# Optimization experiments

Hardware: AMD Instinct MI355X
Metric: run time of the kernel (lower is better)

The kernel has to match this reference:

```python
import jax, jax.numpy as jnp
import numpy as np
from jax import lax

WIN = 11
SIGMA = 1.5


def _gaussian_kernel2d(win_size, channels, dtype):
    g = jnp.arange(win_size, dtype=dtype) - win_size // 2
    g = jnp.exp(-(g ** 2) / (2.0 * SIGMA ** 2))
    g = g / g.sum()
    k2 = jnp.einsum('i,j->ij', g, g)
    return jnp.broadcast_to(k2, (channels, 1, win_size, win_size))


def setup_inputs() -> dict:
    key = jax.random.key(0)
    k1, k2 = jax.random.split(key)
    B, C, H, W = 8, 19, 512, 512
    pred = jax.random.normal(k1, (B, C, H, W), dtype=jnp.float32)
    target = jax.random.randint(k2, (B, H, W), 0, C, dtype=jnp.int64)
    return {"pred": pred, "target": target}


def reference(pred, target):
    B, C, H, W = pred.shape
    win = min(H, W, WIN)
    p = jax.nn.softmax(pred, axis=1)
    t = jax.nn.one_hot(target, C, dtype=p.dtype).transpose(0, 3, 1, 2)  # [B,C,H,W]
    kernel = _gaussian_kernel2d(win, C, p.dtype)

    def dwconv(x):  # depthwise valid conv over all classes at once
        return lax.conv_general_dilated(x, kernel, (1, 1), 'VALID',
                                        feature_group_count=C)

    mu1 = dwconv(p)
    mu2 = dwconv(t)
    mu12 = mu1 * mu2
    mu1sq = mu1 * mu1
    mu2sq = mu2 * mu2
    var1 = dwconv(p * p) - mu1sq
    var2 = dwconv(t * t) - mu2sq
    covar = dwconv(p * t) - mu12

    L = 1.0
    c1 = (0.01 * L) ** 2
    c2 = (0.03 * L) ** 2
    cs = (2.0 * covar + c2) / (var1 + var2 + c2)
    ss = (2.0 * mu12 + c1) / (mu1sq + mu2sq + c1) * cs  # [B,C,H',W']

    ss = ss.reshape(B, C, -1).mean(axis=-1)  # per (batch, class) SSIM
    ss = jax.nn.relu(ss)  # nonnegative=True
    # loss = mean over classes of (1 - mean over batch of ss) == 1 - mean(ss)
    return 1.0 - ss.mean()
```

## Files before the change

kernel.cpp:

```cpp
#include <hip/hip_runtime.h>

namespace {

constexpr int B = 8, C = 19, H = 512, W = 512;
constexpr int OH = 502, OW = 502;
constexpr int HW = H * W;
constexpr int TH = 32, TW = 64;
constexpr int IH = TH + 10, IW = TW + 10;

__device__ constexpr float G[11] = {
    0.00102838f, 0.00759876f, 0.03600077f, 0.10936070f, 0.21300553f,
    0.26601173f,
    0.21300553f, 0.10936070f, 0.03600077f, 0.00759876f, 0.00102838f};

__global__ __launch_bounds__(256) void denom_kernel(
    const float* __restrict__ pred, const int* __restrict__ target,
    float* __restrict__ rs, unsigned char* __restrict__ t8,
    float* __restrict__ accum) {
  int idx = blockIdx.x * 256 + threadIdx.x;
  if (blockIdx.x == 0 && threadIdx.x < B * C) accum[threadIdx.x] = 0.0f;
  if (idx >= B * HW) return;
  int b = idx / HW;
  int px = idx - b * HW;
  const float* pp = pred + (size_t)b * C * HW + px;
  float s = 0.0f;
#pragma unroll
  for (int c = 0; c < C; ++c) s += __expf(pp[c * HW]);
  rs[idx] = 1.0f / s;
  t8[idx] = (unsigned char)target[idx];
}

__global__ __launch_bounds__(256) void ssim_kernel(
    const float* __restrict__ pred, const float* __restrict__ rs,
    const unsigned char* __restrict__ t8, float* __restrict__ accum) {
  __shared__ float sRS[IH][IW];
  __shared__ unsigned char sT[IH][IW];
  __shared__ float sP[IH][IW];
  __shared__ float sH[4][IH][TW];
  __shared__ float red[4];

  const int x0 = blockIdx.x * TW;
  const int y0 = blockIdx.y * TH;
  const int b = blockIdx.z;
  const int ow = min(TW, OW - x0);
  const int oh = min(TH, OH - y0);
  const int iw = ow + 10;
  const int ih = oh + 10;
  const int tid = threadIdx.x;

  for (int i = tid; i < ih * iw; i += 256) {
    int r = i / iw, col = i - r * iw;
    int g = b * HW + (y0 + r) * W + (x0 + col);
    sRS[r][col] = rs[g];
    sT[r][col] = t8[g];
  }
  __syncthreads();

  for (int c = 0; c < C; ++c) {
    const float* pc = pred + (size_t)(b * C + c) * HW;
    for (int i = tid; i < ih * iw; i += 256) {
      int r = i / iw, col = i - r * iw;
      sP[r][col] = __expf(pc[(y0 + r) * W + (x0 + col)]) * sRS[r][col];
    }
    __syncthreads();

    for (int i = tid; i < ih * TW; i += 256) {
      int r = i >> 6;
      int col = i & 63;
      if (col < ow) {
        float hp = 0.f, hp2 = 0.f, hpt = 0.f, ht = 0.f;
#pragma unroll
        for (int j = 0; j < 11; ++j) {
          float v = sP[r][col + j];
          float tf = (sT[r][col + j] == (unsigned char)c) ? 1.0f : 0.0f;
          float gj = G[j];
          hp += gj * v;
          hp2 += gj * v * v;
          hpt += gj * v * tf;
          ht += gj * tf;
        }
        sH[0][r][col] = hp;
        sH[1][r][col] = hp2;
        sH[2][r][col] = hpt;
        sH[3][r][col] = ht;
      }
    }
    __syncthreads();

    float acc = 0.0f;
    for (int i = tid; i < TH * TW; i += 256) {
      int r = i >> 6;
      int col = i & 63;
      if (r < oh && col < ow) {
        float mu1 = 0.f, dp2 = 0.f, dpt = 0.f, mu2 = 0.f;
#pragma unroll
        for (int j = 0; j < 11; ++j) {
          float gj = G[j];
          mu1 += gj * sH[0][r + j][col];
          dp2 += gj * sH[1][r + j][col];
          dpt += gj * sH[2][r + j][col];
          mu2 += gj * sH[3][r + j][col];
        }
        float mu12 = mu1 * mu2;
        float var1 = dp2 - mu1 * mu1;
        float var2 = mu2 - mu2 * mu2;
        float covar = dpt - mu12;
        const float c1 = 1e-4f, c2 = 9e-4f;
        float cs = (2.0f * covar + c2) / (var1 + var2 + c2);
        float ssv = (2.0f * mu12 + c1) / (mu1 * mu1 + mu2 * mu2 + c1) * cs;
        acc += ssv;
      }
    }

    for (int off = 32; off > 0; off >>= 1) acc += __shfl_down(acc, off);
    if ((tid & 63) == 0) red[tid >> 6] = acc;
    __syncthreads();
    if (tid == 0)
      atomicAdd(&accum[b * C + c], red[0] + red[1] + red[2] + red[3]);
  }
}

__global__ __launch_bounds__(256) void finish_kernel(
    const float* __restrict__ accum, float* __restrict__ out) {
  __shared__ float red[4];
  int tid = threadIdx.x;
  float v = 0.0f;
  if (tid < B * C) {
    float m = accum[tid] * (1.0f / (float)(OH * OW));
    v = m > 0.0f ? m : 0.0f;
  }
  for (int off = 32; off > 0; off >>= 1) v += __shfl_down(v, off);
  if ((tid & 63) == 0) red[tid >> 6] = v;
  __syncthreads();
  if (tid == 0) out[0] = 1.0f - (red[0] + red[1] + red[2] + red[3]) /
                                    (float)(B * C);
}

}

extern "C" void kernel_launch(void* const* d_in, const int* in_sizes, int n_in,
                              void* d_out, int out_size, void* d_ws,
                              size_t ws_size, hipStream_t stream) {
  const float* pred = (const float*)d_in[0];
  const int* target = (const int*)d_in[1];
  float* out = (float*)d_out;

  float* rs = (float*)d_ws;
  unsigned char* t8 = (unsigned char*)d_ws + (size_t)B * HW * sizeof(float);
  float* accum = (float*)((char*)d_ws + (size_t)B * HW * 5);

  denom_kernel<<<(B * HW + 255) / 256, 256, 0, stream>>>(pred, target, rs, t8,
                                                         accum);
  dim3 grid((OW + TW - 1) / TW, (OH + TH - 1) / TH, B);
  ssim_kernel<<<grid, 256, 0, stream>>>(pred, rs, t8, accum);
  finish_kernel<<<1, 256, 0, stream>>>(accum, out);
}
```

Measured before the change: 689.2 us.

## Restructure SSIM into register vertical pass, shared horizontal pass, class-split grid

The vertical Gaussian pass now runs in registers: each thread loads an 18-row column strip of pred and keeps rs/target values resident across classes. Only the four vertically filtered maps go through shared memory, and a register-blocked horizontal pass computes 7 outputs per thread. The grid is split four ways over class groups to raise parallelism, the denominator kernel is vectorized with float4/int4, and per-wave atomics replace the block reduction. The cost is a 64-column input tile producing 54 outputs, so more halo reloads, plus higher register pressure under the launch bound of 4 blocks.

```diff
diff --git a/kernel.cpp b/kernel.cpp
--- a/kernel.cpp
+++ b/kernel.cpp
@@ -5,8 +5,13 @@
 constexpr int B = 8, C = 19, H = 512, W = 512;
 constexpr int OH = 502, OW = 502;
 constexpr int HW = H * W;
-constexpr int TH = 32, TW = 64;
-constexpr int IH = TH + 10, IW = TW + 10;
+
+constexpr int TH = 32;
+constexpr int TW = 54;
+constexpr int IW = 64;
+constexpr int RPT = 8;
+constexpr int NJ = RPT + 10;
+constexpr int LW = 68;
 
 __device__ constexpr float G[11] = {
     0.00102838f, 0.00759876f, 0.03600077f, 0.10936070f, 0.21300553f,
@@ -17,106 +22,145 @@
     const float* __restrict__ pred, const int* __restrict__ target,
     float* __restrict__ rs, unsigned char* __restrict__ t8,
     float* __restrict__ accum) {
-  int idx = blockIdx.x * 256 + threadIdx.x;
+  int tid = blockIdx.x * 256 + threadIdx.x;
   if (blockIdx.x == 0 && threadIdx.x < B * C) accum[threadIdx.x] = 0.0f;
-  if (idx >= B * HW) return;
-  int b = idx / HW;
-  int px = idx - b * HW;
-  const float* pp = pred + (size_t)b * C * HW + px;
-  float s = 0.0f;
-#pragma unroll
-  for (int c = 0; c < C; ++c) s += __expf(pp[c * HW]);
-  rs[idx] = 1.0f / s;
-  t8[idx] = (unsigned char)target[idx];
-}
-
-__global__ __launch_bounds__(256) void ssim_kernel(
+  int p4 = tid * 4;
+  int b = p4 / HW;
+  int px = p4 - b * HW;
+  const float4* pp = (const float4*)(pred + (size_t)b * C * HW + px);
+  float4 s = {0.f, 0.f, 0.f, 0.f};
+#pragma unroll
+  for (int c = 0; c < C; ++c) {
+    float4 v = pp[c * (HW / 4)];
+    s.x += __expf(v.x);
+    s.y += __expf(v.y);
+    s.z += __expf(v.z);
+    s.w += __expf(v.w);
+  }
+  float4 r;
+  r.x = 1.0f / s.x;
+  r.y = 1.0f / s.y;
+  r.z = 1.0f / s.z;
+  r.w = 1.0f / s.w;
+  ((float4*)rs)[tid] = r;
+  int4 t = ((const int4*)target)[tid];
+  uchar4 tc;
+  tc.x = (unsigned char)t.x;
+  tc.y = (unsigned char)t.y;
+  tc.z = (unsigned char)t.z;
+  tc.w = (unsigned char)t.w;
+  ((uchar4*)t8)[tid] = tc;
+}
+
+__global__ __launch_bounds__(256, 4) void ssim_kernel(
     const float* __restrict__ pred, const float* __restrict__ rs,
     const unsigned char* __restrict__ t8, float* __restrict__ accum) {
-  __shared__ float sRS[IH][IW];
-  __shared__ unsigned char sT[IH][IW];
-  __shared__ float sP[IH][IW];
-  __shared__ float sH[4][IH][TW];
-  __shared__ float red[4];
-
+  __shared__ float vOut[4][TH][LW];
+
+  const int tid = threadIdx.x;
   const int x0 = blockIdx.x * TW;
   const int y0 = blockIdx.y * TH;
-  const int b = blockIdx.z;
+  const int z = blockIdx.z;
+  const int b = z >> 2;
+  const int c0 = (z & 3) * 5;
+  const int c1 = min(c0 + 5, C);
   const int ow = min(TW, OW - x0);
   const int oh = min(TH, OH - y0);
-  const int iw = ow + 10;
-  const int ih = oh + 10;
-  const int tid = threadIdx.x;
-
-  for (int i = tid; i < ih * iw; i += 256) {
-    int r = i / iw, col = i - r * iw;
-    int g = b * HW + (y0 + r) * W + (x0 + col);
-    sRS[r][col] = rs[g];
-    sT[r][col] = t8[g];
-  }
-  __syncthreads();
-
-  for (int c = 0; c < C; ++c) {
+
+  const int col = tid & 63;
+  const int rg = tid >> 6;
+  const int gc = min(x0 + col, W - 1);
+  const int rbase = y0 + rg * RPT;
+
+  float rsv[NJ];
+  int tv[NJ];
+#pragma unroll
+  for (int j = 0; j < NJ; ++j) {
+    int r = min(rbase + j, H - 1);
+    int o = b * HW + r * W + gc;
+    rsv[j] = rs[o];
+    tv[j] = t8[o];
+  }
+
+  const int prow = tid >> 3;
+  const int cg = tid & 7;
+  const int cbase = cg * 7;
+
+  for (int c = c0; c < c1; ++c) {
+    __syncthreads();
+
     const float* pc = pred + (size_t)(b * C + c) * HW;
-    for (int i = tid; i < ih * iw; i += 256) {
-      int r = i / iw, col = i - r * iw;
-      sP[r][col] = __expf(pc[(y0 + r) * W + (x0 + col)]) * sRS[r][col];
+    float aP[RPT] = {}, aP2[RPT] = {}, aPT[RPT] = {}, aT[RPT] = {};
+#pragma unroll
+    for (int j = 0; j < NJ; ++j) {
+      int r = min(rbase + j, H - 1);
+      float p = __expf(pc[r * W + gc]) * rsv[j];
+      float p2 = p * p;
+      bool hit = (tv[j] == c);
+      float tf = hit ? 1.0f : 0.0f;
+      float pt = hit ? p : 0.0f;
+#pragma unroll
+      for (int o = 0; o < RPT; ++o) {
+        int g = j - o;
+        if (g >= 0 && g < 11) {
+          float gw = G[g];
+          aP[o] = fmaf(gw, p, aP[o]);
+          aP2[o] = fmaf(gw, p2, aP2[o]);
+          aPT[o] = fmaf(gw, pt, aPT[o]);
+          aT[o] = fmaf(gw, tf, aT[o]);
+        }
+      }
+    }
+#pragma unroll
+    for (int o = 0; o < RPT; ++o) {
+      int r = rg * RPT + o;
+      vOut[0][r][col] = aP[o];
+      vOut[1][r][col] = aP2[o];
+      vOut[2][r][col] = aPT[o];
+      vOut[3][r][col] = aT[o];
     }
     __syncthreads();
 
-    for (int i = tid; i < ih * TW; i += 256) {
-      int r = i >> 6;
-      int col = i & 63;
-      if (col < ow) {
-        float hp = 0.f, hp2 = 0.f, hpt = 0.f, ht = 0.f;
-#pragma unroll
-        for (int j = 0; j < 11; ++j) {
-          float v = sP[r][col + j];
-          float tf = (sT[r][col + j] == (unsigned char)c) ? 1.0f : 0.0f;
-          float gj = G[j];
-          hp += gj * v;
-          hp2 += gj * v * v;
-          hpt += gj * v * tf;
-          ht += gj * tf;
+    float mres[4][7];
+#pragma unroll
+    for (int f = 0; f < 4; ++f) {
+      float vin[17];
+#pragma unroll
+      for (int k = 0; k < 17; ++k) vin[k] = vOut[f][prow][cbase + k];
+#pragma unroll
+      for (int o = 0; o < 7; ++o) {
+        float s = 0.0f;
+#pragma unroll
+        for (int j = 0; j < 11; ++j) s = fmaf(G[j], vin[o + j], s);
+        mres[f][o] = s;
+      }
+    }
+
+    float acc = 0.0f;
+    if (prow < oh) {
+#pragma unroll
+      for (int o = 0; o < 7; ++o) {
+        if (cbase + o < ow) {
+          float mu1 = mres[0][o];
+          float dp2 = mres[1][o];
+          float dpt = mres[2][o];
+          float mu2 = mres[3][o];
+          float mu1sq = mu1 * mu1;
+          float mu2sq = mu2 * mu2;
+          float mu12 = mu1 * mu2;
+          float var1 = dp2 - mu1sq;
+          float var2 = mu2 - mu2sq;
+          float covar = dpt - mu12;
+          const float c1c = 1e-4f, c2c = 9e-4f;
+          float num = (2.0f * mu12 + c1c) * (2.0f * covar + c2c);
+          float den = (mu1sq + mu2sq + c1c) * (var1 + var2 + c2c);
+          acc += __fdividef(num, den);
         }
-        sH[0][r][col] = hp;
-        sH[1][r][col] = hp2;
-        sH[2][r][col] = hpt;
-        sH[3][r][col] = ht;
       }
     }
-    __syncthreads();
-
-    float acc = 0.0f;
-    for (int i = tid; i < TH * TW; i += 256) {
-      int r = i >> 6;
-      int col = i & 63;
-      if (r < oh && col < ow) {
-        float mu1 = 0.f, dp2 = 0.f, dpt = 0.f, mu2 = 0.f;
-#pragma unroll
-        for (int j = 0; j < 11; ++j) {
-          float gj = G[j];
-          mu1 += gj * sH[0][r + j][col];
-          dp2 += gj * sH[1][r + j][col];
-          dpt += gj * sH[2][r + j][col];
-          mu2 += gj * sH[3][r + j][col];
-        }
-        float mu12 = mu1 * mu2;
-        float var1 = dp2 - mu1 * mu1;
-        float var2 = mu2 - mu2 * mu2;
-        float covar = dpt - mu12;
-        const float c1 = 1e-4f, c2 = 9e-4f;
-        float cs = (2.0f * covar + c2) / (var1 + var2 + c2);
-        float ssv = (2.0f * mu12 + c1) / (mu1 * mu1 + mu2 * mu2 + c1) * cs;
-        acc += ssv;
-      }
-    }
-
-    for (int off = 32; off > 0; off >>= 1) acc += __shfl_down(acc, off);
-    if ((tid & 63) == 0) red[tid >> 6] = acc;
-    __syncthreads();
-    if (tid == 0)
-      atomicAdd(&accum[b * C + c], red[0] + red[1] + red[2] + red[3]);
+
+    for (int o2 = 32; o2 > 0; o2 >>= 1) acc += __shfl_down(acc, o2);
+    if ((tid & 63) == 0) atomicAdd(&accum[b * C + c], acc);
   }
 }
 
@@ -132,8 +176,8 @@
   for (int off = 32; off > 0; off >>= 1) v += __shfl_down(v, off);
   if ((tid & 63) == 0) red[tid >> 6] = v;
   __syncthreads();
-  if (tid == 0) out[0] = 1.0f - (red[0] + red[1] + red[2] + red[3]) /
-                                    (float)(B * C);
+  if (tid == 0)
+    out[0] = 1.0f - (red[0] + red[1] + red[2] + red[3]) / (float)(B * C);
 }
 
 }
@@ -149,9 +193,8 @@
   unsigned char* t8 = (unsigned char*)d_ws + (size_t)B * HW * sizeof(float);
   float* accum = (float*)((char*)d_ws + (size_t)B * HW * 5);
 
-  denom_kernel<<<(B * HW + 255) / 256, 256, 0, stream>>>(pred, target, rs, t8,
-                                                         accum);
-  dim3 grid((OW + TW - 1) / TW, (OH + TH - 1) / TH, B);
+  denom_kernel<<<B * HW / 1024, 256, 0, stream>>>(pred, target, rs, t8, accum);
+  dim3 grid((OW + TW - 1) / TW, (OH + TH - 1) / TH, B * 4);
   ssim_kernel<<<grid, 256, 0, stream>>>(pred, rs, t8, accum);
   finish_kernel<<<1, 256, 0, stream>>>(accum, out);
 }
```

New measurement: 826.0 us. +19.9%, slower.
